# Kernel tuning notes

Hardware: AMD Instinct MI355X
Metric: run time of the kernel (lower is better)

Reference implementation:

```python
import jax, jax.numpy as jnp
import numpy as np

B, S, D = 2, 2048, 768
HD = 64          # hardcoded head_dim in module
NH = D // HD     # 12 query heads
NKV = max(1, NH // 3)  # 4 kv heads
GROUPS = NH // NKV     # 3
WINDOW = 384
THETA = 10000.0
EPS = 1e-6


def setup_inputs() -> dict:
    key = jax.random.key(0)
    ks = jax.random.split(key, 5)
    return {
        "hidden_states": jax.random.normal(ks[0], (B, S, D), dtype=jnp.float32),
        "q_w": jax.random.normal(ks[1], (NH * HD, D), dtype=jnp.float32) * 0.02,
        "k_w": jax.random.normal(ks[2], (NKV * HD, D), dtype=jnp.float32) * 0.02,
        "v_w": jax.random.normal(ks[3], (NKV * HD, D), dtype=jnp.float32) * 0.02,
        "o_w": jax.random.normal(ks[4], (D, NH * HD), dtype=jnp.float32) * 0.02,
        "q_ln_w": jnp.ones((HD,), dtype=jnp.float32),
        "k_ln_w": jnp.ones((HD,), dtype=jnp.float32),
    }


def _rmsnorm(x, w):
    var = jnp.mean(jnp.square(x.astype(jnp.float32)), axis=-1, keepdims=True)
    return w * (x * jax.lax.rsqrt(var + EPS)).astype(x.dtype)


def _rotate_half(x):
    x1, x2 = jnp.split(x, 2, axis=-1)
    return jnp.concatenate((-x2, x1), axis=-1)


def _rope_cos_sin(seq_len, dtype):
    inv_freq = 1.0 / (THETA ** (jnp.arange(0, HD, 2, dtype=jnp.float32) / HD))
    t = jnp.arange(seq_len, dtype=jnp.float32)
    freqs = jnp.outer(t, inv_freq)            # [S, HD/2]
    emb = jnp.concatenate((freqs, freqs), -1)  # [S, HD]
    return jnp.cos(emb).astype(dtype), jnp.sin(emb).astype(dtype)


def reference(hidden_states, q_w, k_w, v_w, o_w, q_ln_w, k_ln_w):
    b, s, _ = hidden_states.shape
    # projections (nn.Linear: y = x @ W.T)
    q = hidden_states @ q_w.T   # [B,S,NH*HD]
    k = hidden_states @ k_w.T   # [B,S,NKV*HD]
    v = hidden_states @ v_w.T

    q = _rmsnorm(q.reshape(b, s, NH, HD), q_ln_w).transpose(0, 2, 1, 3)      # [B,NH,S,HD]
    k = _rmsnorm(k.reshape(b, s, NKV, HD), k_ln_w).transpose(0, 2, 1, 3)     # [B,NKV,S,HD]
    v = v.reshape(b, s, NKV, HD).transpose(0, 2, 1, 3)                       # [B,NKV,S,HD]

    cos, sin = _rope_cos_sin(s, q.dtype)  # [S,HD]
    cos = cos[None, None]
    sin = sin[None, None]
    q = q * cos + _rotate_half(q) * sin
    k = k * cos + _rotate_half(k) * sin

    # grouped-query repeat: [B,NKV,S,HD] -> [B,NH,S,HD]
    k = jnp.repeat(k, GROUPS, axis=1)
    v = jnp.repeat(v, GROUPS, axis=1)

    scores = jnp.einsum("bhqd,bhkd->bhqk", q, k) / np.sqrt(HD)
    # causal + sliding-window mask: allow i-WINDOW < j <= i
    idx = jnp.arange(s)
    rel = idx[None, :] - idx[:, None]  # j - i
    allowed = (rel <= 0) & (rel > -WINDOW)
    scores = jnp.where(allowed[None, None], scores, -jnp.inf)

    attn = jax.nn.softmax(scores.astype(jnp.float32), axis=-1).astype(q.dtype)
    out = jnp.einsum("bhqk,bhkd->bhqd", attn, v)       # [B,NH,S,HD]
    out = out.transpose(0, 2, 1, 3).reshape(b, s, NH * HD)
    return out @ o_w.T
```

## Files before the change

### kernel.cpp

```cpp
#include <hip/hip_runtime.h>
#include <hip/hip_bf16.h>

typedef __hip_bfloat16 bf16;
typedef __attribute__((ext_vector_type(8))) short bf16x8;
typedef __attribute__((ext_vector_type(4))) float f32x4;
typedef __attribute__((ext_vector_type(16))) float f32x16;

#define MFMA16(a, b, c) __builtin_amdgcn_mfma_f32_16x16x32_bf16((a), (b), (c), 0, 0, 0)
#define MFMA32(a, b, c) __builtin_amdgcn_mfma_f32_32x32x16_bf16((a), (b), (c), 0, 0, 0)


__device__ __forceinline__ void st4bf(bf16* p, float4 v) {
    bf16 t[4];
    t[0] = __float2bfloat16(v.x); t[1] = __float2bfloat16(v.y);
    t[2] = __float2bfloat16(v.z); t[3] = __float2bfloat16(v.w);
    *reinterpret_cast<uint2*>(p) = *reinterpret_cast<const uint2*>(t);
}

__global__ __launch_bounds__(256) void k_prep(
    const float* __restrict__ hs, const float* __restrict__ qw,
    const float* __restrict__ kw, const float* __restrict__ vw,
    const float* __restrict__ ow,
    bf16* __restrict__ hsb, bf16* __restrict__ qwb, bf16* __restrict__ kwb,
    bf16* __restrict__ vwb, bf16* __restrict__ owb, float2* __restrict__ tab)
{
    const int bid = blockIdx.x, tid = threadIdx.x;
    const float* src; bf16* dst; int rel;
    if (bid < 3072)      { src = hs; dst = hsb; rel = bid; }
    else if (bid < 3648) { src = qw; dst = qwb; rel = bid - 3072; }
    else if (bid < 3840) { src = kw; dst = kwb; rel = bid - 3648; }
    else if (bid < 4032) { src = vw; dst = vwb; rel = bid - 3840; }
    else if (bid < 4608) { src = ow; dst = owb; rel = bid - 4032; }
    else {
        int i = (bid - 4608) * 256 + tid;
        int f = i & 31;
        float ang = (float)(i >> 5) * expf(-(float)f * 0.28782313662425572f);
        float sn, cs; sincosf(ang, &sn, &cs);
        tab[i] = make_float2(cs, sn);
        return;
    }
    int i = (rel * 256 + tid) * 4;
    float4 v = *reinterpret_cast<const float4*>(src + i);
    st4bf(dst + i, v);
}

__global__ __launch_bounds__(256) void k_qkv(
    const bf16* __restrict__ hsb, const bf16* __restrict__ qwb,
    const bf16* __restrict__ kwb, const bf16* __restrict__ vwb,
    const float* __restrict__ qln, const float* __restrict__ kln,
    const float2* __restrict__ tab,
    bf16* __restrict__ qo, bf16* __restrict__ ko, bf16* __restrict__ vto)
{
    __shared__ bf16 As[2][64 * 72];
    __shared__ bf16 Bs[2][64 * 72];
    const int tid = threadIdx.x;
    const int w = tid >> 6, l = tid & 63;
    const int lm = l & 15, lg = l >> 4;
    const int m0 = blockIdx.x * 64;
    const int nblk = blockIdx.y;

    const bf16* wsrc; int wrow0, kind, head;
    if (nblk < 12)      { wsrc = qwb; wrow0 = nblk * 64;        kind = 0; head = nblk; }
    else if (nblk < 16) { wsrc = kwb; wrow0 = (nblk - 12) * 64; kind = 1; head = nblk - 12; }
    else                { wsrc = vwb; wrow0 = (nblk - 16) * 64; kind = 2; head = nblk - 16; }

    const int sr = tid >> 2, sc = (tid & 3) * 16;
    const bf16* aptr = hsb  + (size_t)(m0 + sr) * 768 + sc;
    const bf16* bptr = wsrc + (size_t)(wrow0 + sr) * 768 + sc;

    bf16x8 rA0 = *(const bf16x8*)(aptr);
    bf16x8 rA1 = *(const bf16x8*)(aptr + 8);
    bf16x8 rA2 = *(const bf16x8*)(bptr);
    bf16x8 rA3 = *(const bf16x8*)(bptr + 8);
    bf16x8 rB0 = *(const bf16x8*)(aptr + 64);
    bf16x8 rB1 = *(const bf16x8*)(aptr + 72);
    bf16x8 rB2 = *(const bf16x8*)(bptr + 64);
    bf16x8 rB3 = *(const bf16x8*)(bptr + 72);

    f32x4 acc[4] = {};
    for (int t = 0; t < 12; ++t) {
        const int p = t & 1;
        *(bf16x8*)(&As[p][sr * 72 + sc])     = rA0;
        *(bf16x8*)(&As[p][sr * 72 + sc + 8]) = rA1;
        *(bf16x8*)(&Bs[p][sr * 72 + sc])     = rA2;
        *(bf16x8*)(&Bs[p][sr * 72 + sc + 8]) = rA3;
        __syncthreads();
        rA0 = rB0; rA1 = rB1; rA2 = rB2; rA3 = rB3;
        if (t < 10) {
            const int off = (t + 2) * 64;
            rB0 = *(const bf16x8*)(aptr + off);
            rB1 = *(const bf16x8*)(aptr + off + 8);
            rB2 = *(const bf16x8*)(bptr + off);
            rB3 = *(const bf16x8*)(bptr + off + 8);
        }
        #pragma unroll
        for (int kk = 0; kk < 2; ++kk) {
            bf16x8 af = *(const bf16x8*)(&As[p][(w * 16 + lm) * 72 + kk * 32 + lg * 8]);
            #pragma unroll
            for (int ct = 0; ct < 4; ++ct) {
                bf16x8 bfr = *(const bf16x8*)(&Bs[p][(ct * 16 + lm) * 72 + kk * 32 + lg * 8]);
                acc[ct] = MFMA16(af, bfr, acc[ct]);
            }
        }
    }

    const int b  = m0 >> 11;
    const int s0 = m0 & 2047;

    if (kind == 2) {
        bf16* base = vto + (size_t)(b * 4 + head) * 64 * 2048;
        #pragma unroll
        for (int r = 0; r < 4; ++r) {
            const int s = s0 + w * 16 + lg * 4 + r;
            #pragma unroll
            for (int ct = 0; ct < 4; ++ct)
                base[(size_t)(ct * 16 + lm) * 2048 + s] = __float2bfloat16(acc[ct][r]);
        }
        return;
    }

    const float* ln = (kind == 0) ? qln : kln;
    const float qscl = (kind == 0) ? 0.18033688011117042f : 1.0f;
    float lw[4];
    #pragma unroll
    for (int ct = 0; ct < 4; ++ct) lw[ct] = ln[ct * 16 + lm] * qscl;

    bf16* base = (kind == 0) ? qo + ((size_t)(b * 12 + head) * 2048 + s0) * 64
                             : ko + ((size_t)(b * 4  + head) * 2048 + s0) * 64;
    #pragma unroll
    for (int r = 0; r < 4; ++r) {
        float n0 = acc[0][r], n1 = acc[1][r], n2 = acc[2][r], n3 = acc[3][r];
        float ss = n0 * n0 + n1 * n1 + n2 * n2 + n3 * n3;
        ss += __shfl_xor(ss, 1);
        ss += __shfl_xor(ss, 2);
        ss += __shfl_xor(ss, 4);
        ss += __shfl_xor(ss, 8);
        float rms = rsqrtf(ss * (1.0f / 64.0f) + 1e-6f);
        n0 *= rms * lw[0]; n1 *= rms * lw[1]; n2 *= rms * lw[2]; n3 *= rms * lw[3];
        const int row = w * 16 + lg * 4 + r;
        const float2* tp = tab + (size_t)(s0 + row) * 32;
        float2 t0 = tp[lm], t1 = tp[lm + 16];
        bf16* dst = base + (size_t)row * 64;
        dst[lm]      = __float2bfloat16(n0 * t0.x - n2 * t0.y);
        dst[lm + 16] = __float2bfloat16(n1 * t1.x - n3 * t1.y);
        dst[lm + 32] = __float2bfloat16(n2 * t0.x + n0 * t0.y);
        dst[lm + 48] = __float2bfloat16(n3 * t1.x + n1 * t1.y);
    }
}

__global__ __launch_bounds__(128) void k_attn(
    const bf16* __restrict__ qi, const bf16* __restrict__ ki,
    const bf16* __restrict__ vti, bf16* __restrict__ ao)
{
    __shared__ bf16 Ks[2][64 * 72];
    __shared__ bf16 Vs[2][64 * 72];
    const int tid = threadIdx.x;
    const int w = tid >> 6, l = tid & 63;
    const int p = l >> 5, c31 = l & 31;
    const int qb = blockIdx.x, h = blockIdx.y, b = blockIdx.z;
    const int kv = h / 3;
    const int q0 = qb * 64;
    const int qw0 = q0 + w * 32;
    const int q_g = qw0 + c31;

    const bf16* qrow = qi + ((size_t)((b * 12 + h) * 2048 + q_g)) * 64 + p * 8;
    bf16x8 qf0 = *(const bf16x8*)(qrow);
    bf16x8 qf1 = *(const bf16x8*)(qrow + 16);
    bf16x8 qf2 = *(const bf16x8*)(qrow + 32);
    bf16x8 qf3 = *(const bf16x8*)(qrow + 48);

    f32x16 oacc0 = {}, oacc1 = {};
    float m_ = -INFINITY, l_ = 0.f;

    const int sr = tid >> 1, sc = (tid & 1) * 32;
    const bf16* kgb = ki  + (size_t)(b * 4 + kv) * 2048 * 64;
    const bf16* vgb = vti + (size_t)(b * 4 + kv) * 64 * 2048;

    const int kb_lo = (qb > 6) ? (qb - 6) : 0;
    bf16x8 rk[4], rv[4];
    {
        const bf16* kp = kgb + (size_t)(kb_lo * 64 + sr) * 64 + sc;
        const bf16* vp = vgb + (size_t)sr * 2048 + kb_lo * 64 + sc;
        #pragma unroll
        for (int j = 0; j < 4; ++j) {
            rk[j] = *(const bf16x8*)(kp + j * 8);
            rv[j] = *(const bf16x8*)(vp + j * 8);
        }
    }

    for (int kb = kb_lo; kb <= qb; ++kb) {
        const int pb = (kb - kb_lo) & 1;
        const int k0 = kb * 64;

        #pragma unroll
        for (int j = 0; j < 4; ++j) {
            *(bf16x8*)(&Ks[pb][sr * 72 + sc + j * 8]) = rk[j];
            *(bf16x8*)(&Vs[pb][sr * 72 + sc + j * 8]) = rv[j];
        }
        __syncthreads();
        if (kb < qb) {
            const bf16* kp = kgb + (size_t)(k0 + 64 + sr) * 64 + sc;
            const bf16* vp = vgb + (size_t)sr * 2048 + k0 + 64 + sc;
            #pragma unroll
            for (int j = 0; j < 4; ++j) {
                rk[j] = *(const bf16x8*)(kp + j * 8);
                rv[j] = *(const bf16x8*)(vp + j * 8);
            }
        }

        f32x16 s0 = {}, s1 = {};
        {
            const bf16* kbase = &Ks[pb][c31 * 72 + p * 8];
            s0 = MFMA32(*(const bf16x8*)(kbase),      qf0, s0);
            s0 = MFMA32(*(const bf16x8*)(kbase + 16), qf1, s0);
            s0 = MFMA32(*(const bf16x8*)(kbase + 32), qf2, s0);
            s0 = MFMA32(*(const bf16x8*)(kbase + 48), qf3, s0);
            const bf16* kbase1 = kbase + 32 * 72;
            s1 = MFMA32(*(const bf16x8*)(kbase1),      qf0, s1);
            s1 = MFMA32(*(const bf16x8*)(kbase1 + 16), qf1, s1);
            s1 = MFMA32(*(const bf16x8*)(kbase1 + 32), qf2, s1);
            s1 = MFMA32(*(const bf16x8*)(kbase1 + 48), qf3, s1);
        }

        const bool need_mask = (64 * kb + 63 > qw0) || (64 * kb <= qw0 - 353);
        if (need_mask) {
            #pragma unroll
            for (int r = 0; r < 16; ++r) {
                int kl = (r & 3) + 8 * (r >> 2) + 4 * p;
                int kg0 = k0 + kl, kg1 = k0 + 32 + kl;
                bool ok0 = (kg0 <= q_g) && (kg0 > q_g - 384);
                bool ok1 = (kg1 <= q_g) && (kg1 > q_g - 384);
                s0[r] = ok0 ? s0[r] : -INFINITY;
                s1[r] = ok1 ? s1[r] : -INFINITY;
            }
        }

        float tm[16];
        #pragma unroll
        for (int i = 0; i < 16; ++i) tm[i] = fmaxf(s0[i], s1[i]);
        #pragma unroll
        for (int st = 8; st > 0; st >>= 1)
            #pragma unroll
            for (int i = 0; i < st; ++i) tm[i] = fmaxf(tm[i], tm[i + st]);
        float tmax = fmaxf(tm[0], __shfl_xor(tm[0], 32));

        float mnew = fmaxf(m_, tmax);
        float scale, rs;
        if (mnew > -INFINITY) {
            scale = exp2f(m_ - mnew);
            #pragma unroll
            for (int r = 0; r < 16; ++r) { s0[r] = exp2f(s0[r] - mnew); }
            #pragma unroll
            for (int r = 0; r < 16; ++r) { s1[r] = exp2f(s1[r] - mnew); }
            float su[16];
            #pragma unroll
            for (int i = 0; i < 16; ++i) su[i] = s0[i] + s1[i];
            #pragma unroll
            for (int st = 8; st > 0; st >>= 1)
                #pragma unroll
                for (int i = 0; i < st; ++i) su[i] += su[i + st];
            rs = su[0];
        } else {
            scale = 1.f;
            rs = 0.f;
            #pragma unroll
            for (int r = 0; r < 16; ++r) { s0[r] = 0.f; s1[r] = 0.f; }
        }
        m_ = mnew;
        rs += __shfl_xor(rs, 32);
        l_ = l_ * scale + rs;
        #pragma unroll
        for (int r = 0; r < 16; ++r) { oacc0[r] *= scale; oacc1[r] *= scale; }

        bf16x8 paf[4];
        #pragma unroll
        for (int kt = 0; kt < 2; ++kt) {
            unsigned pk[8];
            #pragma unroll
            for (int i = 0; i < 8; ++i) {
                float lo = (kt == 0) ? s0[2 * i] : s1[2 * i];
                float hi = (kt == 0) ? s0[2 * i + 1] : s1[2 * i + 1];
                bf16 blo = __float2bfloat16(lo), bhi = __float2bfloat16(hi);
                pk[i] = ((unsigned)*(unsigned short*)&bhi << 16) | (unsigned)*(unsigned short*)&blo;
            }
            unsigned x[8];
            #pragma unroll
            for (int i = 0; i < 8; ++i) x[i] = (unsigned)__shfl_xor((int)pk[i], 32);
            #pragma unroll
            for (int s = 0; s < 2; ++s) {
                union { int4 i4; bf16x8 v; } u;
                u.i4.x = p ? (int)x[4 * s + 2] : (int)pk[4 * s];
                u.i4.y = p ? (int)x[4 * s + 3] : (int)pk[4 * s + 1];
                u.i4.z = p ? (int)pk[4 * s + 2] : (int)x[4 * s];
                u.i4.w = p ? (int)pk[4 * s + 3] : (int)x[4 * s + 1];
                paf[kt * 2 + s] = u.v;
            }
        }

        {
            const bf16* vbase = &Vs[pb][c31 * 72 + p * 8];
            oacc0 = MFMA32(*(const bf16x8*)(vbase),      paf[0], oacc0);
            oacc0 = MFMA32(*(const bf16x8*)(vbase + 16), paf[1], oacc0);
            oacc0 = MFMA32(*(const bf16x8*)(vbase + 32), paf[2], oacc0);
            oacc0 = MFMA32(*(const bf16x8*)(vbase + 48), paf[3], oacc0);
            const bf16* vbase1 = vbase + 32 * 72;
            oacc1 = MFMA32(*(const bf16x8*)(vbase1),      paf[0], oacc1);
            oacc1 = MFMA32(*(const bf16x8*)(vbase1 + 16), paf[1], oacc1);
            oacc1 = MFMA32(*(const bf16x8*)(vbase1 + 32), paf[2], oacc1);
            oacc1 = MFMA32(*(const bf16x8*)(vbase1 + 48), paf[3], oacc1);
        }
    }

    const float inv = 1.f / l_;
    bf16* dst = ao + ((size_t)(b * 2048 + q_g)) * 768 + h * 64;
    #pragma unroll
    for (int g = 0; g < 4; ++g) {
        union { uint2 u2; bf16 t[4]; } o0, o1;
        #pragma unroll
        for (int e = 0; e < 4; ++e) {
            o0.t[e] = __float2bfloat16(oacc0[4 * g + e] * inv);
            o1.t[e] = __float2bfloat16(oacc1[4 * g + e] * inv);
        }
        *reinterpret_cast<uint2*>(dst + 8 * g + 4 * p)      = o0.u2;
        *reinterpret_cast<uint2*>(dst + 32 + 8 * g + 4 * p) = o1.u2;
    }
}

__global__ __launch_bounds__(256) void k_oproj(
    const bf16* __restrict__ A, const bf16* __restrict__ W, float* __restrict__ out)
{
    __shared__ bf16 As[2][64 * 72];
    __shared__ bf16 Bs[2][64 * 72];
    const int tid = threadIdx.x;
    const int w = tid >> 6, l = tid & 63;
    const int lm = l & 15, lg = l >> 4;
    const int m0 = blockIdx.x * 64, n0 = blockIdx.y * 64;

    const int sr = tid >> 2, sc = (tid & 3) * 16;
    const bf16* aptr = A + (size_t)(m0 + sr) * 768 + sc;
    const bf16* bptr = W + (size_t)(n0 + sr) * 768 + sc;

    bf16x8 rA0 = *(const bf16x8*)(aptr);
    bf16x8 rA1 = *(const bf16x8*)(aptr + 8);
    bf16x8 rA2 = *(const bf16x8*)(bptr);
    bf16x8 rA3 = *(const bf16x8*)(bptr + 8);
    bf16x8 rB0 = *(const bf16x8*)(aptr + 64);
    bf16x8 rB1 = *(const bf16x8*)(aptr + 72);
    bf16x8 rB2 = *(const bf16x8*)(bptr + 64);
    bf16x8 rB3 = *(const bf16x8*)(bptr + 72);

    f32x4 acc[4] = {};
    for (int t = 0; t < 12; ++t) {
        const int p = t & 1;
        *(bf16x8*)(&As[p][sr * 72 + sc])     = rA0;
        *(bf16x8*)(&As[p][sr * 72 + sc + 8]) = rA1;
        *(bf16x8*)(&Bs[p][sr * 72 + sc])     = rA2;
        *(bf16x8*)(&Bs[p][sr * 72 + sc + 8]) = rA3;
        __syncthreads();
        rA0 = rB0; rA1 = rB1; rA2 = rB2; rA3 = rB3;
        if (t < 10) {
            const int off = (t + 2) * 64;
            rB0 = *(const bf16x8*)(aptr + off);
            rB1 = *(const bf16x8*)(aptr + off + 8);
            rB2 = *(const bf16x8*)(bptr + off);
            rB3 = *(const bf16x8*)(bptr + off + 8);
        }
        #pragma unroll
        for (int kk = 0; kk < 2; ++kk) {
            bf16x8 af = *(const bf16x8*)(&As[p][(w * 16 + lm) * 72 + kk * 32 + lg * 8]);
            #pragma unroll
            for (int ct = 0; ct < 4; ++ct) {
                bf16x8 bfr = *(const bf16x8*)(&Bs[p][(ct * 16 + lm) * 72 + kk * 32 + lg * 8]);
                acc[ct] = MFMA16(af, bfr, acc[ct]);
            }
        }
    }

    #pragma unroll
    for (int r = 0; r < 4; ++r) {
        float* dst = out + (size_t)(m0 + w * 16 + lg * 4 + r) * 768 + n0;
        #pragma unroll
        for (int ct = 0; ct < 4; ++ct)
            dst[ct * 16 + lm] = acc[ct][r];
    }
}

extern "C" void kernel_launch(void* const* d_in, const int* in_sizes, int n_in,
                              void* d_out, int out_size, void* d_ws, size_t ws_size,
                              hipStream_t stream) {
    const float* hs  = (const float*)d_in[0];
    const float* qw  = (const float*)d_in[1];
    const float* kw  = (const float*)d_in[2];
    const float* vw  = (const float*)d_in[3];
    const float* ow  = (const float*)d_in[4];
    const float* qln = (const float*)d_in[5];
    const float* kln = (const float*)d_in[6];
    float* out = (float*)d_out;

    float2* tab  = (float2*)d_ws;
    bf16*   q_ws = (bf16*)(tab + 65536);
    bf16*   k_ws = q_ws + 3145728;
    bf16*   vt_ws= k_ws + 1048576;
    bf16*   x_ws = vt_ws + 1048576;
    bf16*   qwb  = x_ws + 3145728;
    bf16*   kwb  = qwb + 589824;
    bf16*   vwb  = kwb + 196608;
    bf16*   owb  = vwb + 196608;

    k_prep<<<dim3(4864), 256, 0, stream>>>(hs, qw, kw, vw, ow, x_ws, qwb, kwb, vwb, owb, tab);
    k_qkv<<<dim3(64, 20, 1), 256, 0, stream>>>(x_ws, qwb, kwb, vwb, qln, kln, tab, q_ws, k_ws, vt_ws);
    k_attn<<<dim3(32, 12, 2), 128, 0, stream>>>(q_ws, k_ws, vt_ws, x_ws);
    k_oproj<<<dim3(64, 12, 1), 256, 0, stream>>>(x_ws, owb, out);
}
```

Before: 64.22 us.

## Split attention KV range across two waves per query tile, load K/V directly into registers

Each block now handles 32 queries and its two waves split the KV tiles between them. Each wave keeps its own online-softmax state, and the two partial results are merged through shared memory at the end. K/V fragments are loaded straight from global memory into registers with next-tile prefetch, which removes the shared-memory staging and the per-iteration barrier. The grid doubles to give more blocks and finer split-K parallelism. The cost is extra global K/V traffic, since there is no reuse across waves, plus a merge step.

```diff
diff --git a/kernel.cpp b/kernel.cpp
--- a/kernel.cpp
+++ b/kernel.cpp
@@ -152,16 +152,14 @@
     const bf16* __restrict__ qi, const bf16* __restrict__ ki,
     const bf16* __restrict__ vti, bf16* __restrict__ ao)
 {
-    __shared__ bf16 Ks[2][64 * 72];
-    __shared__ bf16 Vs[2][64 * 72];
+    __shared__ float pbuf[64 * 34];
     const int tid = threadIdx.x;
     const int w = tid >> 6, l = tid & 63;
     const int p = l >> 5, c31 = l & 31;
-    const int qb = blockIdx.x, h = blockIdx.y, b = blockIdx.z;
+    const int qs0 = blockIdx.x * 32;
+    const int h = blockIdx.y, b = blockIdx.z;
     const int kv = h / 3;
-    const int q0 = qb * 64;
-    const int qw0 = q0 + w * 32;
-    const int q_g = qw0 + c31;
+    const int q_g = qs0 + c31;
 
     const bf16* qrow = qi + ((size_t)((b * 12 + h) * 2048 + q_g)) * 64 + p * 8;
     bf16x8 qf0 = *(const bf16x8*)(qrow);
@@ -169,60 +167,55 @@
     bf16x8 qf2 = *(const bf16x8*)(qrow + 32);
     bf16x8 qf3 = *(const bf16x8*)(qrow + 48);
 
+    const bf16* kgb = ki  + (size_t)(b * 4 + kv) * 2048 * 64;
+    const bf16* vgb = vti + (size_t)(b * 4 + kv) * 64 * 2048;
+
+    const int kb_lo = (qs0 >= 384) ? ((qs0 - 383) >> 6) : 0;
+    const int kb_hi = (qs0 + 31) >> 6;
+    const int nt = kb_hi - kb_lo + 1;
+    const int n0 = nt >> 1;
+    const int kb_s = w ? kb_lo + n0 : kb_lo;
+    const int kb_e = w ? kb_hi : kb_lo + n0 - 1;
+
     f32x16 oacc0 = {}, oacc1 = {};
     float m_ = -INFINITY, l_ = 0.f;
 
-    const int sr = tid >> 1, sc = (tid & 1) * 32;
-    const bf16* kgb = ki  + (size_t)(b * 4 + kv) * 2048 * 64;
-    const bf16* vgb = vti + (size_t)(b * 4 + kv) * 64 * 2048;
-
-    const int kb_lo = (qb > 6) ? (qb - 6) : 0;
-    bf16x8 rk[4], rv[4];
-    {
-        const bf16* kp = kgb + (size_t)(kb_lo * 64 + sr) * 64 + sc;
-        const bf16* vp = vgb + (size_t)sr * 2048 + kb_lo * 64 + sc;
+    bf16x8 kf[8], vf[8];
+    if (kb_s <= kb_e) {
+        const bf16* kb0 = kgb + ((size_t)(kb_s * 64 + c31)) * 64 + p * 8;
+        const bf16* vb0 = vgb + (size_t)c31 * 2048 + kb_s * 64 + p * 8;
         #pragma unroll
         for (int j = 0; j < 4; ++j) {
-            rk[j] = *(const bf16x8*)(kp + j * 8);
-            rv[j] = *(const bf16x8*)(vp + j * 8);
-        }
-    }
-
-    for (int kb = kb_lo; kb <= qb; ++kb) {
-        const int pb = (kb - kb_lo) & 1;
+            kf[j]     = *(const bf16x8*)(kb0 + j * 16);
+            kf[4 + j] = *(const bf16x8*)(kb0 + 32 * 64 + j * 16);
+            vf[j]     = *(const bf16x8*)(vb0 + j * 16);
+            vf[4 + j] = *(const bf16x8*)(vb0 + 32 * 2048 + j * 16);
+        }
+    }
+
+    for (int kb = kb_s; kb <= kb_e; ++kb) {
         const int k0 = kb * 64;
 
-        #pragma unroll
-        for (int j = 0; j < 4; ++j) {
-            *(bf16x8*)(&Ks[pb][sr * 72 + sc + j * 8]) = rk[j];
-            *(bf16x8*)(&Vs[pb][sr * 72 + sc + j * 8]) = rv[j];
-        }
-        __syncthreads();
-        if (kb < qb) {
-            const bf16* kp = kgb + (size_t)(k0 + 64 + sr) * 64 + sc;
-            const bf16* vp = vgb + (size_t)sr * 2048 + k0 + 64 + sc;
+        f32x16 s0 = {}, s1 = {};
+        s0 = MFMA32(kf[0], qf0, s0);
+        s0 = MFMA32(kf[1], qf1, s0);
+        s0 = MFMA32(kf[2], qf2, s0);
+        s0 = MFMA32(kf[3], qf3, s0);
+        s1 = MFMA32(kf[4], qf0, s1);
+        s1 = MFMA32(kf[5], qf1, s1);
+        s1 = MFMA32(kf[6], qf2, s1);
+        s1 = MFMA32(kf[7], qf3, s1);
+
+        if (kb < kb_e) {
+            const bf16* kbn = kgb + ((size_t)((kb + 1) * 64 + c31)) * 64 + p * 8;
             #pragma unroll
             for (int j = 0; j < 4; ++j) {
-                rk[j] = *(const bf16x8*)(kp + j * 8);
-                rv[j] = *(const bf16x8*)(vp + j * 8);
-            }
-        }
-
-        f32x16 s0 = {}, s1 = {};
-        {
-            const bf16* kbase = &Ks[pb][c31 * 72 + p * 8];
-            s0 = MFMA32(*(const bf16x8*)(kbase),      qf0, s0);
-            s0 = MFMA32(*(const bf16x8*)(kbase + 16), qf1, s0);
-            s0 = MFMA32(*(const bf16x8*)(kbase + 32), qf2, s0);
-            s0 = MFMA32(*(const bf16x8*)(kbase + 48), qf3, s0);
-            const bf16* kbase1 = kbase + 32 * 72;
-            s1 = MFMA32(*(const bf16x8*)(kbase1),      qf0, s1);
-            s1 = MFMA32(*(const bf16x8*)(kbase1 + 16), qf1, s1);
-            s1 = MFMA32(*(const bf16x8*)(kbase1 + 32), qf2, s1);
-            s1 = MFMA32(*(const bf16x8*)(kbase1 + 48), qf3, s1);
-        }
-
-        const bool need_mask = (64 * kb + 63 > qw0) || (64 * kb <= qw0 - 353);
+                kf[j]     = *(const bf16x8*)(kbn + j * 16);
+                kf[4 + j] = *(const bf16x8*)(kbn + 32 * 64 + j * 16);
+            }
+        }
+
+        const bool need_mask = (64 * kb + 63 > qs0) || (64 * kb <= qs0 - 353);
         if (need_mask) {
             #pragma unroll
             for (int r = 0; r < 16; ++r) {
@@ -297,32 +290,52 @@
             }
         }
 
-        {
-            const bf16* vbase = &Vs[pb][c31 * 72 + p * 8];
-            oacc0 = MFMA32(*(const bf16x8*)(vbase),      paf[0], oacc0);
-            oacc0 = MFMA32(*(const bf16x8*)(vbase + 16), paf[1], oacc0);
-            oacc0 = MFMA32(*(const bf16x8*)(vbase + 32), paf[2], oacc0);
-            oacc0 = MFMA32(*(const bf16x8*)(vbase + 48), paf[3], oacc0);
-            const bf16* vbase1 = vbase + 32 * 72;
-            oacc1 = MFMA32(*(const bf16x8*)(vbase1),      paf[0], oacc1);
-            oacc1 = MFMA32(*(const bf16x8*)(vbase1 + 16), paf[1], oacc1);
-            oacc1 = MFMA32(*(const bf16x8*)(vbase1 + 32), paf[2], oacc1);
-            oacc1 = MFMA32(*(const bf16x8*)(vbase1 + 48), paf[3], oacc1);
-        }
-    }
-
-    const float inv = 1.f / l_;
-    bf16* dst = ao + ((size_t)(b * 2048 + q_g)) * 768 + h * 64;
-    #pragma unroll
-    for (int g = 0; g < 4; ++g) {
-        union { uint2 u2; bf16 t[4]; } o0, o1;
-        #pragma unroll
-        for (int e = 0; e < 4; ++e) {
-            o0.t[e] = __float2bfloat16(oacc0[4 * g + e] * inv);
-            o1.t[e] = __float2bfloat16(oacc1[4 * g + e] * inv);
-        }
-        *reinterpret_cast<uint2*>(dst + 8 * g + 4 * p)      = o0.u2;
-        *reinterpret_cast<uint2*>(dst + 32 + 8 * g + 4 * p) = o1.u2;
+        oacc0 = MFMA32(vf[0], paf[0], oacc0);
+        oacc0 = MFMA32(vf[1], paf[1], oacc0);
+        oacc0 = MFMA32(vf[2], paf[2], oacc0);
+        oacc0 = MFMA32(vf[3], paf[3], oacc0);
+        oacc1 = MFMA32(vf[4], paf[0], oacc1);
+        oacc1 = MFMA32(vf[5], paf[1], oacc1);
+        oacc1 = MFMA32(vf[6], paf[2], oacc1);
+        oacc1 = MFMA32(vf[7], paf[3], oacc1);
+
+        if (kb < kb_e) {
+            const bf16* vbn = vgb + (size_t)c31 * 2048 + (kb + 1) * 64 + p * 8;
+            #pragma unroll
+            for (int j = 0; j < 4; ++j) {
+                vf[j]     = *(const bf16x8*)(vbn + j * 16);
+                vf[4 + j] = *(const bf16x8*)(vbn + 32 * 2048 + j * 16);
+            }
+        }
+    }
+
+    if (w == 1) {
+        float* pb = pbuf + l * 34;
+        #pragma unroll
+        for (int r = 0; r < 16; ++r) { pb[r] = oacc0[r]; pb[16 + r] = oacc1[r]; }
+        pb[32] = m_;
+        pb[33] = l_;
+    }
+    __syncthreads();
+    if (w == 0) {
+        const float* pb = pbuf + l * 34;
+        const float m1 = pb[32], l1 = pb[33];
+        const float mm = fmaxf(m_, m1);
+        const float sc0 = (m_ > -INFINITY) ? exp2f(m_ - mm) : 0.f;
+        const float sc1 = (m1 > -INFINITY) ? exp2f(m1 - mm) : 0.f;
+        const float inv = 1.f / (l_ * sc0 + l1 * sc1);
+        bf16* dst = ao + ((size_t)(b * 2048 + q_g)) * 768 + h * 64;
+        #pragma unroll
+        for (int g = 0; g < 4; ++g) {
+            union { uint2 u2; bf16 t[4]; } o0, o1;
+            #pragma unroll
+            for (int e = 0; e < 4; ++e) {
+                o0.t[e] = __float2bfloat16((oacc0[4 * g + e] * sc0 + pb[4 * g + e] * sc1) * inv);
+                o1.t[e] = __float2bfloat16((oacc1[4 * g + e] * sc0 + pb[16 + 4 * g + e] * sc1) * inv);
+            }
+            *reinterpret_cast<uint2*>(dst + 8 * g + 4 * p)      = o0.u2;
+            *reinterpret_cast<uint2*>(dst + 32 + 8 * g + 4 * p) = o1.u2;
+        }
     }
 }
 
@@ -409,6 +422,6 @@
 
     k_prep<<<dim3(4864), 256, 0, stream>>>(hs, qw, kw, vw, ow, x_ws, qwb, kwb, vwb, owb, tab);
     k_qkv<<<dim3(64, 20, 1), 256, 0, stream>>>(x_ws, qwb, kwb, vwb, qln, kln, tab, q_ws, k_ws, vt_ws);
-    k_attn<<<dim3(32, 12, 2), 128, 0, stream>>>(q_ws, k_ws, vt_ws, x_ws);
+    k_attn<<<dim3(64, 12, 2), 128, 0, stream>>>(q_ws, k_ws, vt_ws, x_ws);
     k_oproj<<<dim3(64, 12, 1), 256, 0, stream>>>(x_ws, owb, out);
 }
```

After: 71.20 us. +10.9%, slower.

## Process two KV tiles per attention iteration with one softmax rescale

Applied to the files above, without the earlier changes.

The attention loop now loads and stages two 64-key K/V tiles per iteration into both LDS buffers. It computes scores for 128 keys, does one online-softmax max/rescale step for them, and runs both PV MFMA groups together. The aim is to halve the per-tile barrier, rescale and reduction overhead and to give more MFMA work between syncs. It also wraps the MFMA blocks in s_setprio. In exchange it doubles the prefetch registers and drops the overlap from the old ping-pong buffers, since a second barrier now ends each iteration. It also pads odd tile counts with a masked duplicate tile.

```diff
diff --git a/kernel.cpp b/kernel.cpp
--- a/kernel.cpp
+++ b/kernel.cpp
@@ -177,67 +177,112 @@
     const bf16* vgb = vti + (size_t)(b * 4 + kv) * 64 * 2048;
 
     const int kb_lo = (qb > 6) ? (qb - 6) : 0;
-    bf16x8 rk[4], rv[4];
+
+    bf16x8 rk[8], rv[8];
     {
-        const bf16* kp = kgb + (size_t)(kb_lo * 64 + sr) * 64 + sc;
-        const bf16* vp = vgb + (size_t)sr * 2048 + kb_lo * 64 + sc;
+        const int t1s = (kb_lo + 1 <= qb) ? kb_lo + 1 : qb;
+        const bf16* kp0 = kgb + (size_t)(kb_lo * 64 + sr) * 64 + sc;
+        const bf16* vp0 = vgb + (size_t)sr * 2048 + kb_lo * 64 + sc;
+        const bf16* kp1 = kgb + (size_t)(t1s * 64 + sr) * 64 + sc;
+        const bf16* vp1 = vgb + (size_t)sr * 2048 + t1s * 64 + sc;
         #pragma unroll
         for (int j = 0; j < 4; ++j) {
-            rk[j] = *(const bf16x8*)(kp + j * 8);
-            rv[j] = *(const bf16x8*)(vp + j * 8);
-        }
-    }
-
-    for (int kb = kb_lo; kb <= qb; ++kb) {
-        const int pb = (kb - kb_lo) & 1;
-        const int k0 = kb * 64;
+            rk[j]     = *(const bf16x8*)(kp0 + j * 8);
+            rv[j]     = *(const bf16x8*)(vp0 + j * 8);
+            rk[4 + j] = *(const bf16x8*)(kp1 + j * 8);
+            rv[4 + j] = *(const bf16x8*)(vp1 + j * 8);
+        }
+    }
+
+    for (int t0 = kb_lo; t0 <= qb; t0 += 2) {
+        const bool t1valid = (t0 + 1 <= qb);
+        const int k00 = t0 * 64, k01 = (t0 + 1) * 64;
 
         #pragma unroll
         for (int j = 0; j < 4; ++j) {
-            *(bf16x8*)(&Ks[pb][sr * 72 + sc + j * 8]) = rk[j];
-            *(bf16x8*)(&Vs[pb][sr * 72 + sc + j * 8]) = rv[j];
+            *(bf16x8*)(&Ks[0][sr * 72 + sc + j * 8]) = rk[j];
+            *(bf16x8*)(&Vs[0][sr * 72 + sc + j * 8]) = rv[j];
+            *(bf16x8*)(&Ks[1][sr * 72 + sc + j * 8]) = rk[4 + j];
+            *(bf16x8*)(&Vs[1][sr * 72 + sc + j * 8]) = rv[4 + j];
         }
         __syncthreads();
-        if (kb < qb) {
-            const bf16* kp = kgb + (size_t)(k0 + 64 + sr) * 64 + sc;
-            const bf16* vp = vgb + (size_t)sr * 2048 + k0 + 64 + sc;
+
+        if (t0 + 2 <= qb) {
+            const int n0t = t0 + 2;
+            const int n1s = (n0t + 1 <= qb) ? n0t + 1 : qb;
+            const bf16* kp0 = kgb + (size_t)(n0t * 64 + sr) * 64 + sc;
+            const bf16* vp0 = vgb + (size_t)sr * 2048 + n0t * 64 + sc;
+            const bf16* kp1 = kgb + (size_t)(n1s * 64 + sr) * 64 + sc;
+            const bf16* vp1 = vgb + (size_t)sr * 2048 + n1s * 64 + sc;
             #pragma unroll
             for (int j = 0; j < 4; ++j) {
-                rk[j] = *(const bf16x8*)(kp + j * 8);
-                rv[j] = *(const bf16x8*)(vp + j * 8);
-            }
-        }
-
-        f32x16 s0 = {}, s1 = {};
+                rk[j]     = *(const bf16x8*)(kp0 + j * 8);
+                rv[j]     = *(const bf16x8*)(vp0 + j * 8);
+                rk[4 + j] = *(const bf16x8*)(kp1 + j * 8);
+                rv[4 + j] = *(const bf16x8*)(vp1 + j * 8);
+            }
+        }
+
+        f32x16 s0 = {}, s1 = {}, s2 = {}, s3 = {};
+        __builtin_amdgcn_s_setprio(1);
         {
-            const bf16* kbase = &Ks[pb][c31 * 72 + p * 8];
-            s0 = MFMA32(*(const bf16x8*)(kbase),      qf0, s0);
-            s0 = MFMA32(*(const bf16x8*)(kbase + 16), qf1, s0);
-            s0 = MFMA32(*(const bf16x8*)(kbase + 32), qf2, s0);
-            s0 = MFMA32(*(const bf16x8*)(kbase + 48), qf3, s0);
-            const bf16* kbase1 = kbase + 32 * 72;
-            s1 = MFMA32(*(const bf16x8*)(kbase1),      qf0, s1);
-            s1 = MFMA32(*(const bf16x8*)(kbase1 + 16), qf1, s1);
-            s1 = MFMA32(*(const bf16x8*)(kbase1 + 32), qf2, s1);
-            s1 = MFMA32(*(const bf16x8*)(kbase1 + 48), qf3, s1);
-        }
-
-        const bool need_mask = (64 * kb + 63 > qw0) || (64 * kb <= qw0 - 353);
-        if (need_mask) {
+            const bf16* ka = &Ks[0][c31 * 72 + p * 8];
+            s0 = MFMA32(*(const bf16x8*)(ka),      qf0, s0);
+            s0 = MFMA32(*(const bf16x8*)(ka + 16), qf1, s0);
+            s0 = MFMA32(*(const bf16x8*)(ka + 32), qf2, s0);
+            s0 = MFMA32(*(const bf16x8*)(ka + 48), qf3, s0);
+            const bf16* kb1 = ka + 32 * 72;
+            s1 = MFMA32(*(const bf16x8*)(kb1),      qf0, s1);
+            s1 = MFMA32(*(const bf16x8*)(kb1 + 16), qf1, s1);
+            s1 = MFMA32(*(const bf16x8*)(kb1 + 32), qf2, s1);
+            s1 = MFMA32(*(const bf16x8*)(kb1 + 48), qf3, s1);
+            const bf16* kc = &Ks[1][c31 * 72 + p * 8];
+            s2 = MFMA32(*(const bf16x8*)(kc),      qf0, s2);
+            s2 = MFMA32(*(const bf16x8*)(kc + 16), qf1, s2);
+            s2 = MFMA32(*(const bf16x8*)(kc + 32), qf2, s2);
+            s2 = MFMA32(*(const bf16x8*)(kc + 48), qf3, s2);
+            const bf16* kd = kc + 32 * 72;
+            s3 = MFMA32(*(const bf16x8*)(kd),      qf0, s3);
+            s3 = MFMA32(*(const bf16x8*)(kd + 16), qf1, s3);
+            s3 = MFMA32(*(const bf16x8*)(kd + 32), qf2, s3);
+            s3 = MFMA32(*(const bf16x8*)(kd + 48), qf3, s3);
+        }
+        __builtin_amdgcn_s_setprio(0);
+
+        const bool nm0 = (64 * t0 + 63 > qw0) || (64 * t0 <= qw0 - 353);
+        if (nm0) {
             #pragma unroll
             for (int r = 0; r < 16; ++r) {
                 int kl = (r & 3) + 8 * (r >> 2) + 4 * p;
-                int kg0 = k0 + kl, kg1 = k0 + 32 + kl;
+                int kg0 = k00 + kl, kg1 = k00 + 32 + kl;
                 bool ok0 = (kg0 <= q_g) && (kg0 > q_g - 384);
                 bool ok1 = (kg1 <= q_g) && (kg1 > q_g - 384);
                 s0[r] = ok0 ? s0[r] : -INFINITY;
                 s1[r] = ok1 ? s1[r] : -INFINITY;
             }
         }
+        if (!t1valid) {
+            #pragma unroll
+            for (int r = 0; r < 16; ++r) { s2[r] = -INFINITY; s3[r] = -INFINITY; }
+        } else {
+            const bool nm1 = (64 * (t0 + 1) + 63 > qw0) || (64 * (t0 + 1) <= qw0 - 353);
+            if (nm1) {
+                #pragma unroll
+                for (int r = 0; r < 16; ++r) {
+                    int kl = (r & 3) + 8 * (r >> 2) + 4 * p;
+                    int kg0 = k01 + kl, kg1 = k01 + 32 + kl;
+                    bool ok0 = (kg0 <= q_g) && (kg0 > q_g - 384);
+                    bool ok1 = (kg1 <= q_g) && (kg1 > q_g - 384);
+                    s2[r] = ok0 ? s2[r] : -INFINITY;
+                    s3[r] = ok1 ? s3[r] : -INFINITY;
+                }
+            }
+        }
 
         float tm[16];
         #pragma unroll
-        for (int i = 0; i < 16; ++i) tm[i] = fmaxf(s0[i], s1[i]);
+        for (int i = 0; i < 16; ++i)
+            tm[i] = fmaxf(fmaxf(s0[i], s1[i]), fmaxf(s2[i], s3[i]));
         #pragma unroll
         for (int st = 8; st > 0; st >>= 1)
             #pragma unroll
@@ -252,9 +297,13 @@
             for (int r = 0; r < 16; ++r) { s0[r] = exp2f(s0[r] - mnew); }
             #pragma unroll
             for (int r = 0; r < 16; ++r) { s1[r] = exp2f(s1[r] - mnew); }
+            #pragma unroll
+            for (int r = 0; r < 16; ++r) { s2[r] = exp2f(s2[r] - mnew); }
+            #pragma unroll
+            for (int r = 0; r < 16; ++r) { s3[r] = exp2f(s3[r] - mnew); }
             float su[16];
             #pragma unroll
-            for (int i = 0; i < 16; ++i) su[i] = s0[i] + s1[i];
+            for (int i = 0; i < 16; ++i) su[i] = (s0[i] + s1[i]) + (s2[i] + s3[i]);
             #pragma unroll
             for (int st = 8; st > 0; st >>= 1)
                 #pragma unroll
@@ -264,7 +313,7 @@
             scale = 1.f;
             rs = 0.f;
             #pragma unroll
-            for (int r = 0; r < 16; ++r) { s0[r] = 0.f; s1[r] = 0.f; }
+            for (int r = 0; r < 16; ++r) { s0[r] = 0.f; s1[r] = 0.f; s2[r] = 0.f; s3[r] = 0.f; }
         }
         m_ = mnew;
         rs += __shfl_xor(rs, 32);
@@ -272,43 +321,61 @@
         #pragma unroll
         for (int r = 0; r < 16; ++r) { oacc0[r] *= scale; oacc1[r] *= scale; }
 
-        bf16x8 paf[4];
-        #pragma unroll
-        for (int kt = 0; kt < 2; ++kt) {
-            unsigned pk[8];
-            #pragma unroll
-            for (int i = 0; i < 8; ++i) {
-                float lo = (kt == 0) ? s0[2 * i] : s1[2 * i];
-                float hi = (kt == 0) ? s0[2 * i + 1] : s1[2 * i + 1];
-                bf16 blo = __float2bfloat16(lo), bhi = __float2bfloat16(hi);
-                pk[i] = ((unsigned)*(unsigned short*)&bhi << 16) | (unsigned)*(unsigned short*)&blo;
-            }
-            unsigned x[8];
-            #pragma unroll
-            for (int i = 0; i < 8; ++i) x[i] = (unsigned)__shfl_xor((int)pk[i], 32);
-            #pragma unroll
-            for (int s = 0; s < 2; ++s) {
-                union { int4 i4; bf16x8 v; } u;
-                u.i4.x = p ? (int)x[4 * s + 2] : (int)pk[4 * s];
-                u.i4.y = p ? (int)x[4 * s + 3] : (int)pk[4 * s + 1];
-                u.i4.z = p ? (int)pk[4 * s + 2] : (int)x[4 * s];
-                u.i4.w = p ? (int)pk[4 * s + 3] : (int)x[4 * s + 1];
-                paf[kt * 2 + s] = u.v;
-            }
-        }
-
+        bf16x8 paf[4], paf2[4];
+        #pragma unroll
+        for (int sl = 0; sl < 2; ++sl) {
+            #pragma unroll
+            for (int kt = 0; kt < 2; ++kt) {
+                unsigned pk[8], x[8];
+                #pragma unroll
+                for (int i = 0; i < 8; ++i) {
+                    float lo, hi;
+                    if (sl == 0) { lo = (kt == 0) ? s0[2 * i] : s1[2 * i];
+                                   hi = (kt == 0) ? s0[2 * i + 1] : s1[2 * i + 1]; }
+                    else         { lo = (kt == 0) ? s2[2 * i] : s3[2 * i];
+                                   hi = (kt == 0) ? s2[2 * i + 1] : s3[2 * i + 1]; }
+                    bf16 blo = __float2bfloat16(lo), bhi = __float2bfloat16(hi);
+                    pk[i] = ((unsigned)*(unsigned short*)&bhi << 16) | (unsigned)*(unsigned short*)&blo;
+                }
+                #pragma unroll
+                for (int i = 0; i < 8; ++i) x[i] = (unsigned)__shfl_xor((int)pk[i], 32);
+                #pragma unroll
+                for (int s = 0; s < 2; ++s) {
+                    union { int4 i4; bf16x8 v; } u;
+                    u.i4.x = p ? (int)x[4 * s + 2] : (int)pk[4 * s];
+                    u.i4.y = p ? (int)x[4 * s + 3] : (int)pk[4 * s + 1];
+                    u.i4.z = p ? (int)pk[4 * s + 2] : (int)x[4 * s];
+                    u.i4.w = p ? (int)pk[4 * s + 3] : (int)x[4 * s + 1];
+                    if (sl == 0) paf[kt * 2 + s] = u.v; else paf2[kt * 2 + s] = u.v;
+                }
+            }
+        }
+
+        __builtin_amdgcn_s_setprio(1);
         {
-            const bf16* vbase = &Vs[pb][c31 * 72 + p * 8];
-            oacc0 = MFMA32(*(const bf16x8*)(vbase),      paf[0], oacc0);
-            oacc0 = MFMA32(*(const bf16x8*)(vbase + 16), paf[1], oacc0);
-            oacc0 = MFMA32(*(const bf16x8*)(vbase + 32), paf[2], oacc0);
-            oacc0 = MFMA32(*(const bf16x8*)(vbase + 48), paf[3], oacc0);
-            const bf16* vbase1 = vbase + 32 * 72;
-            oacc1 = MFMA32(*(const bf16x8*)(vbase1),      paf[0], oacc1);
-            oacc1 = MFMA32(*(const bf16x8*)(vbase1 + 16), paf[1], oacc1);
-            oacc1 = MFMA32(*(const bf16x8*)(vbase1 + 32), paf[2], oacc1);
-            oacc1 = MFMA32(*(const bf16x8*)(vbase1 + 48), paf[3], oacc1);
-        }
+            const bf16* va = &Vs[0][c31 * 72 + p * 8];
+            oacc0 = MFMA32(*(const bf16x8*)(va),      paf[0], oacc0);
+            oacc0 = MFMA32(*(const bf16x8*)(va + 16), paf[1], oacc0);
+            oacc0 = MFMA32(*(const bf16x8*)(va + 32), paf[2], oacc0);
+            oacc0 = MFMA32(*(const bf16x8*)(va + 48), paf[3], oacc0);
+            const bf16* vb = va + 32 * 72;
+            oacc1 = MFMA32(*(const bf16x8*)(vb),      paf[0], oacc1);
+            oacc1 = MFMA32(*(const bf16x8*)(vb + 16), paf[1], oacc1);
+            oacc1 = MFMA32(*(const bf16x8*)(vb + 32), paf[2], oacc1);
+            oacc1 = MFMA32(*(const bf16x8*)(vb + 48), paf[3], oacc1);
+            const bf16* vc = &Vs[1][c31 * 72 + p * 8];
+            oacc0 = MFMA32(*(const bf16x8*)(vc),      paf2[0], oacc0);
+            oacc0 = MFMA32(*(const bf16x8*)(vc + 16), paf2[1], oacc0);
+            oacc0 = MFMA32(*(const bf16x8*)(vc + 32), paf2[2], oacc0);
+            oacc0 = MFMA32(*(const bf16x8*)(vc + 48), paf2[3], oacc0);
+            const bf16* vd = vc + 32 * 72;
+            oacc1 = MFMA32(*(const bf16x8*)(vd),      paf2[0], oacc1);
+            oacc1 = MFMA32(*(const bf16x8*)(vd + 16), paf2[1], oacc1);
+            oacc1 = MFMA32(*(const bf16x8*)(vd + 32), paf2[2], oacc1);
+            oacc1 = MFMA32(*(const bf16x8*)(vd + 48), paf2[3], oacc1);
+        }
+        __builtin_amdgcn_s_setprio(0);
+        __syncthreads();
     }
 
     const float inv = 1.f / l_;
```

Measured after the change: 76.60 us. 19.3% more time.
